# Performance work log

Measured on AMD Instinct MI355X. Metric: run time of the kernel, lower is better.

The kernel has to match this reference:

```python
import jax, jax.numpy as jnp
import numpy as np

B, N, M, K = 128, 128, 16, 8      # graphs, nodes/graph, num_samples, pearl_k
H_MLP = 16                        # pearl_mlp_out
D_PE = 64                         # pe_dims (GIN hidden/out)
E = 262144
BN_EPS = 1e-5


def setup_inputs() -> dict:
    key = jax.random.key(0)
    ks = jax.random.split(key, 16)
    lap = jax.random.normal(ks[0], (B, N, N), dtype=jnp.float32) * 0.1
    W0 = jax.random.normal(ks[1], (B, N, M), dtype=jnp.float32)
    edge_index = jax.random.randint(ks[2], (2, E), 0, B * N, dtype=jnp.int32)
    s = lambda k, sh, fan: jax.random.normal(k, sh, dtype=jnp.float32) / np.sqrt(fan)
    return {
        "lap": lap,
        "W0": W0,
        "mlp_W": s(ks[3], (K, H_MLP), K),
        "mlp_b": jnp.zeros((H_MLP,), jnp.float32),
        "bn_g": jnp.ones((H_MLP,), jnp.float32),
        "bn_b": jnp.zeros((H_MLP,), jnp.float32),
        "eps1": jnp.zeros((), jnp.float32),
        "W1a": s(ks[4], (H_MLP, D_PE), H_MLP),
        "b1a": jnp.zeros((D_PE,), jnp.float32),
        "W1b": s(ks[5], (D_PE, D_PE), D_PE),
        "b1b": jnp.zeros((D_PE,), jnp.float32),
        "eps2": jnp.zeros((), jnp.float32),
        "W2a": s(ks[6], (D_PE, D_PE), D_PE),
        "b2a": jnp.zeros((D_PE,), jnp.float32),
        "W2b": s(ks[7], (D_PE, D_PE), D_PE),
        "b2b": jnp.zeros((D_PE,), jnp.float32),
        "edge_index": edge_index,
    }


def _gin_layer(h, eps, Wa, ba, Wb, bb, src, dst, num_nodes):
    # h: [Nsum, M, D]; GIN aggregation: (1+eps)*h + sum_{j in N(i)} h_j
    agg = jax.ops.segment_sum(h[src], dst, num_segments=num_nodes)
    z = (1.0 + eps) * h + agg
    z = jax.nn.relu(jnp.einsum("nmd,de->nme", z, Wa) + ba)
    z = jnp.einsum("nmd,de->nme", z, Wb) + bb
    return jax.nn.relu(z)


def reference(lap, W0, mlp_W, mlp_b, bn_g, bn_b, eps1, W1a, b1a, W1b, b1b,
              eps2, W2a, b2a, W2b, b2b, edge_index):
    # polynomial filter: stack [W, S@W, S^2@W, ...]  -> [B, N, M, K]
    out = W0
    ws = [out]
    for _ in range(K - 1):
        out = jnp.einsum("bij,bjm->bim", lap, out)
        ws.append(out)
    feat = jnp.stack(ws, axis=-1)                       # [B, N, M, K]

    # per-graph MLP over trailing k dim + BatchNorm1d (training stats, per graph)
    h = jnp.einsum("bnmk,kh->bnmh", feat, mlp_W) + mlp_b  # [B, N, M, H]
    mu = jnp.mean(h, axis=(1, 2), keepdims=True)
    var = jnp.var(h, axis=(1, 2), keepdims=True)
    h = (h - mu) * jax.lax.rsqrt(var + BN_EPS) * bn_g + bn_b
    h = jax.nn.relu(h)

    # concat graphs -> [Nsum, M, H]; GIN over batched edge_index
    h = h.reshape(B * N, M, H_MLP)
    src, dst = edge_index[0], edge_index[1]
    h = _gin_layer(h, eps1, W1a, b1a, W1b, b1b, src, dst, B * N)
    h = _gin_layer(h, eps2, W2a, b2a, W2b, b2b, src, dst, B * N)

    # RandomSampleAggregator: sum over the sample dim -> [Nsum, D_pe]
    return h.sum(axis=1)
```

## Files before the change

### kernel.cpp

```cpp
#include <hip/hip_runtime.h>

typedef unsigned short u16;
typedef unsigned int   u32;
typedef short bf16x8 __attribute__((ext_vector_type(8)));
typedef float f32x4  __attribute__((ext_vector_type(4)));

#define BG    128
#define NN    128
#define MS    16
#define KP    8
#define HM    16
#define DP    64
#define NSUM  16384
#define NE    262144
#define SITES 2048


__device__ __forceinline__ float blo(u32 u){ union{u32 i; float f;} v; v.i=u<<16; return v.f; }
__device__ __forceinline__ float bhi(u32 u){ union{u32 i; float f;} v; v.i=u&0xffff0000u; return v.f; }
__device__ __forceinline__ u16  f2b(float f){ union{float f; u32 i;} v; v.f=f; u32 x=v.i; x += 0x7fffu + ((x>>16)&1u); return (u16)(x>>16); }
__device__ __forceinline__ u32  pk2(float a, float b){ return (u32)f2b(a) | ((u32)f2b(b)<<16); }

__device__ __forceinline__ void fsplit(float x, short& hi, short& lo){
  u16 h = f2b(x); hi = (short)h; lo = (short)f2b(x - blo((u32)h));
}

__device__ __forceinline__ void acc4s(float* a, uint2 x, float s){
  a[0]+=s*blo(x.x); a[1]+=s*bhi(x.x); a[2]+=s*blo(x.y); a[3]+=s*bhi(x.y);
}
__device__ __forceinline__ void acc16s(float* a, uint4 x0, uint4 x1, float s){
  a[0] +=s*blo(x0.x); a[1] +=s*bhi(x0.x); a[2] +=s*blo(x0.y); a[3] +=s*bhi(x0.y);
  a[4] +=s*blo(x0.z); a[5] +=s*bhi(x0.z); a[6] +=s*blo(x0.w); a[7] +=s*bhi(x0.w);
  a[8] +=s*blo(x1.x); a[9] +=s*bhi(x1.x); a[10]+=s*blo(x1.y); a[11]+=s*bhi(x1.y);
  a[12]+=s*blo(x1.z); a[13]+=s*bhi(x1.z); a[14]+=s*blo(x1.w); a[15]+=s*bhi(x1.w);
}

#define MFMA16(a,b,c) __builtin_amdgcn_mfma_f32_16x16x32_bf16(a,b,c,0,0,0)

__device__ __forceinline__ bf16x8 bfragW(const float* __restrict__ W, int nrows,
                                         int k0, int nb, int col, int quad){
  bf16x8 f;
  #pragma unroll
  for(int j=0;j<8;++j){
    int k = k0 + quad*8 + j;
    float v = (k < nrows) ? W[k*DP + nb + col] : 0.f;
    f[j] = (short)f2b(v);
  }
  return f;
}
__device__ __forceinline__ bf16x8 afragT(const float* tp){
  float4 v0 = *(const float4*)tp;
  float4 v1 = *(const float4*)(tp+4);
  bf16x8 a;
  a[0]=(short)f2b(v0.x); a[1]=(short)f2b(v0.y); a[2]=(short)f2b(v0.z); a[3]=(short)f2b(v0.w);
  a[4]=(short)f2b(v1.x); a[5]=(short)f2b(v1.y); a[6]=(short)f2b(v1.z); a[7]=(short)f2b(v1.w);
  return a;
}

__global__ __launch_bounds__(256,1) void k_poly(
    const float* __restrict__ lap, const float* __restrict__ W0, const float* __restrict__ mlpW,
    const float* __restrict__ bng, const float* __restrict__ bnb, u16* __restrict__ h1,
    int* __restrict__ cnt)
{
  __shared__ float Wbuf[2][SITES];
  __shared__ float mlpWS[KP*HM];
  __shared__ float red[4][32];
  __shared__ float stat[32];
  __shared__ float ssc[HM], ssh[HM];

  const int b = blockIdx.x, t = threadIdx.x, l = t&63, w = t>>6;
  const int col = l&15, quad = l>>4;
  if (t < 128) cnt[b*128 + t] = 0;

  {
    const float4* src = (const float4*)(W0 + (size_t)b*SITES);
    for (int i=t; i<SITES/4; i+=256) ((float4*)Wbuf[0])[i] = src[i];
    if (t < KP*HM) mlpWS[t] = mlpW[t];
  }

  bf16x8 Ah[2][4], Al[2][4];
  {
    const float* lg = lap + (size_t)b*NN*NN;
    #pragma unroll
    for(int Mt=0;Mt<2;++Mt){
      const int nr = w*32 + Mt*16 + col;
      #pragma unroll
      for(int Kc=0;Kc<4;++Kc){
        const float* p = lg + (size_t)nr*NN + Kc*32 + quad*8;
        float4 v0 = *(const float4*)p;
        float4 v1 = *(const float4*)(p+4);
        float xs[8] = {v0.x,v0.y,v0.z,v0.w,v1.x,v1.y,v1.z,v1.w};
        #pragma unroll
        for(int j=0;j<8;++j){ short hi,lo; fsplit(xs[j],hi,lo); Ah[Mt][Kc][j]=hi; Al[Mt][Kc][j]=lo; }
      }
    }
  }

  float h[8][16];
  {
    const float* w0g = W0 + (size_t)b*SITES;
    #pragma unroll
    for(int Mt=0;Mt<2;++Mt){
      #pragma unroll
      for(int r=0;r<4;++r){
        const int n = w*32 + Mt*16 + quad*4 + r;
        float sv = w0g[n*MS + col];
        #pragma unroll
        for(int c=0;c<16;++c) h[Mt*4+r][c] = sv*mlpW[c];
      }
    }
  }
  __syncthreads();

  int cur=0;
  for(int k=1;k<KP;++k){
    f32x4 c0 = {0.f,0.f,0.f,0.f};
    f32x4 c1 = {0.f,0.f,0.f,0.f};
    #pragma unroll
    for(int Kc=0;Kc<4;++Kc){
      const float* wb = &Wbuf[cur][(Kc*32 + quad*8)*MS + col];
      bf16x8 Bh, Bl;
      #pragma unroll
      for(int j=0;j<8;++j){
        float x = wb[j*MS];
        short hi,lo; fsplit(x,hi,lo); Bh[j]=hi; Bl[j]=lo;
      }
      c0 = MFMA16(Ah[0][Kc], Bh, c0);
      c0 = MFMA16(Ah[0][Kc], Bl, c0);
      c0 = MFMA16(Al[0][Kc], Bh, c0);
      c1 = MFMA16(Ah[1][Kc], Bh, c1);
      c1 = MFMA16(Ah[1][Kc], Bl, c1);
      c1 = MFMA16(Al[1][Kc], Bh, c1);
    }
    float mw[16];
    #pragma unroll
    for(int c=0;c<16;++c) mw[c]=mlpWS[k*16+c];
    #pragma unroll
    for(int r=0;r<4;++r){
      const int n0 = w*32 + quad*4 + r;
      Wbuf[cur^1][n0*MS + col]        = c0[r];
      Wbuf[cur^1][(n0+16)*MS + col]   = c1[r];
      #pragma unroll
      for(int c=0;c<16;++c){ h[r][c] += c0[r]*mw[c]; h[4+r][c] += c1[r]*mw[c]; }
    }
    __syncthreads();
    cur ^= 1;
  }

  float sum[16], sq[16];
  #pragma unroll
  for(int c=0;c<16;++c){ sum[c]=0.f; sq[c]=0.f; }
  #pragma unroll
  for(int s=0;s<8;++s){
    #pragma unroll
    for(int c=0;c<16;++c){ float v=h[s][c]; sum[c]+=v; sq[c]+=v*v; }
  }
  #pragma unroll
  for(int d=1;d<64;d<<=1){
    #pragma unroll
    for(int c=0;c<16;++c){ sum[c]+=__shfl_xor(sum[c],d,64); sq[c]+=__shfl_xor(sq[c],d,64); }
  }
  if(l==0){
    #pragma unroll
    for(int c=0;c<16;++c){ red[w][c]=sum[c]; red[w][16+c]=sq[c]; }
  }
  __syncthreads();
  if(t<32) stat[t]=red[0][t]+red[1][t]+red[2][t]+red[3][t];
  __syncthreads();
  if(t<16){
    float mu  = stat[t]*(1.f/SITES);
    float var = stat[16+t]*(1.f/SITES) - mu*mu;
    float sc  = bng[t] * rsqrtf(var + 1e-5f);
    ssc[t]=sc; ssh[t]=bnb[t] - mu*sc;
  }
  __syncthreads();
  {
    float sc[16], sh[16];
    #pragma unroll
    for(int c=0;c<16;++c){ sc[c]=ssc[c]; sh[c]=ssh[c]; }
    #pragma unroll
    for(int s=0;s<8;++s){
      const int n = w*32 + (s>>2)*16 + quad*4 + (s&3);
      const int node = b*NN + n;
      float r[16];
      #pragma unroll
      for(int c=0;c<16;++c) r[c]=fmaxf(h[s][c]*sc[c]+sh[c], 0.f);
      uint4 A;
      A.x=pk2(r[0],r[1]);  A.y=pk2(r[2],r[3]);  A.z=pk2(r[4],r[5]);  A.w=pk2(r[6],r[7]);
      uint4 Bv;
      Bv.x=pk2(r[8],r[9]); Bv.y=pk2(r[10],r[11]); Bv.z=pk2(r[12],r[13]); Bv.w=pk2(r[14],r[15]);
      u16* o = h1 + (size_t)node*256 + (size_t)col*HM;
      *(uint4*)o     = A;
      *(uint4*)(o+8) = Bv;
    }
  }
}

__global__ void k_hist(const int* __restrict__ dst, int* __restrict__ cnt){
  int e = blockIdx.x*256 + threadIdx.x;
  atomicAdd(&cnt[dst[e]], 1);
}

__global__ void k_scan(const int* __restrict__ cnt, int* __restrict__ off, int* __restrict__ wpos){
  __shared__ int ps[256];
  const int t = threadIdx.x, PER = NSUM/256;
  int s=0;
  for(int i=0;i<PER;++i) s += cnt[t*PER+i];
  ps[t]=s; __syncthreads();
  for(int d=1; d<256; d<<=1){
    int v = (t>=d) ? ps[t-d] : 0;
    __syncthreads();
    ps[t] += v;
    __syncthreads();
  }
  int run = (t==0) ? 0 : ps[t-1];
  for(int i=0;i<PER;++i){
    int idx=t*PER+i;
    off[idx]=run; wpos[idx]=run;
    run += cnt[idx];
  }
  if(t==255) off[NSUM]=run;
}

__global__ void k_scatter(const int* __restrict__ srcI, const int* __restrict__ dstI,
                          int* __restrict__ wpos, int* __restrict__ srcs){
  int e = blockIdx.x*256 + threadIdx.x;
  int p = atomicAdd(&wpos[dstI[e]], 1);
  srcs[p] = srcI[e];
}

__global__ __launch_bounds__(256) void k_agg1(
  const u16* __restrict__ h1, const float* __restrict__ eps1p,
  const int* __restrict__ off, const int* __restrict__ srcs, u16* __restrict__ z1)
{
  const int t=threadIdx.x, l=t&63;
  const int node = blockIdx.x*4 + (t>>6);
  const float epe = 1.f + eps1p[0];
  float a[4] = {0.f,0.f,0.f,0.f};
  acc4s(a, *(const uint2*)&h1[(size_t)node*256 + l*4], epe);
  int e=off[node]; const int e1=off[node+1];
  for(; e+8<=e1; e+=8){
    int s0=srcs[e],s1=srcs[e+1],s2=srcs[e+2],s3=srcs[e+3];
    int s4=srcs[e+4],s5=srcs[e+5],s6=srcs[e+6],s7=srcs[e+7];
    uint2 r0=*(const uint2*)&h1[(size_t)s0*256 + l*4];
    uint2 r1=*(const uint2*)&h1[(size_t)s1*256 + l*4];
    uint2 r2=*(const uint2*)&h1[(size_t)s2*256 + l*4];
    uint2 r3=*(const uint2*)&h1[(size_t)s3*256 + l*4];
    uint2 r4=*(const uint2*)&h1[(size_t)s4*256 + l*4];
    uint2 r5=*(const uint2*)&h1[(size_t)s5*256 + l*4];
    uint2 r6=*(const uint2*)&h1[(size_t)s6*256 + l*4];
    uint2 r7=*(const uint2*)&h1[(size_t)s7*256 + l*4];
    acc4s(a,r0,1.f); acc4s(a,r1,1.f); acc4s(a,r2,1.f); acc4s(a,r3,1.f);
    acc4s(a,r4,1.f); acc4s(a,r5,1.f); acc4s(a,r6,1.f); acc4s(a,r7,1.f);
  }
  for(; e<e1; ++e){
    uint2 r=*(const uint2*)&h1[(size_t)srcs[e]*256 + l*4];
    acc4s(a,r,1.f);
  }
  uint2 o; o.x=pk2(a[0],a[1]); o.y=pk2(a[2],a[3]);
  *(uint2*)&z1[(size_t)node*256 + l*4] = o;
}

__global__ __launch_bounds__(256) void k_agg2(
  const u16* __restrict__ h2, const float* __restrict__ eps2p,
  const int* __restrict__ off, const int* __restrict__ srcs, u16* __restrict__ z2)
{
  const int t=threadIdx.x, l=t&63;
  const int node = blockIdx.x*4 + (t>>6);
  const float epe = 1.f + eps2p[0];
  float a[16];
  #pragma unroll
  for(int i=0;i<16;++i) a[i]=0.f;
  {
    const uint4* r=(const uint4*)&h2[(size_t)node*1024 + l*16];
    acc16s(a, r[0], r[1], epe);
  }
  int e=off[node]; const int e1=off[node+1];
  for(; e+8<=e1; e+=8){
    int s0=srcs[e],s1=srcs[e+1],s2=srcs[e+2],s3=srcs[e+3];
    int s4=srcs[e+4],s5=srcs[e+5],s6=srcs[e+6],s7=srcs[e+7];
    const uint4* r0=(const uint4*)&h2[(size_t)s0*1024 + l*16];
    const uint4* r1=(const uint4*)&h2[(size_t)s1*1024 + l*16];
    const uint4* r2=(const uint4*)&h2[(size_t)s2*1024 + l*16];
    const uint4* r3=(const uint4*)&h2[(size_t)s3*1024 + l*16];
    const uint4* r4=(const uint4*)&h2[(size_t)s4*1024 + l*16];
    const uint4* r5=(const uint4*)&h2[(size_t)s5*1024 + l*16];
    const uint4* r6=(const uint4*)&h2[(size_t)s6*1024 + l*16];
    const uint4* r7=(const uint4*)&h2[(size_t)s7*1024 + l*16];
    uint4 a0=r0[0],b0=r0[1], a1=r1[0],b1=r1[1], a2=r2[0],b2=r2[1], a3=r3[0],b3=r3[1];
    uint4 a4=r4[0],b4=r4[1], a5=r5[0],b5=r5[1], a6=r6[0],b6=r6[1], a7=r7[0],b7=r7[1];
    acc16s(a,a0,b0,1.f); acc16s(a,a1,b1,1.f); acc16s(a,a2,b2,1.f); acc16s(a,a3,b3,1.f);
    acc16s(a,a4,b4,1.f); acc16s(a,a5,b5,1.f); acc16s(a,a6,b6,1.f); acc16s(a,a7,b7,1.f);
  }
  for(; e<e1; ++e){
    const uint4* r=(const uint4*)&h2[(size_t)srcs[e]*1024 + l*16];
    acc16s(a, r[0], r[1], 1.f);
  }
  uint4 o0, o1;
  o0.x=pk2(a[0],a[1]);   o0.y=pk2(a[2],a[3]);   o0.z=pk2(a[4],a[5]);   o0.w=pk2(a[6],a[7]);
  o1.x=pk2(a[8],a[9]);   o1.y=pk2(a[10],a[11]); o1.z=pk2(a[12],a[13]); o1.w=pk2(a[14],a[15]);
  uint4* zp = (uint4*)&z2[(size_t)node*1024 + l*16];
  zp[0]=o0; zp[1]=o1;
}

__global__ __launch_bounds__(256) void k_mm1(
  const u16* __restrict__ z1, const float* __restrict__ W1a, const float* __restrict__ b1a,
  const float* __restrict__ W1b, const float* __restrict__ b1b, u16* __restrict__ h2)
{
  __shared__ float tS[4][16*68 + 4];
  const int t=threadIdx.x, l=t&63, w=t>>6;
  const int col=l&15, quad=l>>4;

  bf16x8 fa[4], fb[4][2];
  float bav[4], bbv[4];
  #pragma unroll
  for(int nt=0;nt<4;++nt){
    fa[nt]    = bfragW(W1a, HM, 0,  nt*16, col, quad);
    fb[nt][0] = bfragW(W1b, DP, 0,  nt*16, col, quad);
    fb[nt][1] = bfragW(W1b, DP, 32, nt*16, col, quad);
    bav[nt] = b1a[nt*16+col];
    bbv[nt] = b1b[nt*16+col];
  }
  for(int ni=0;ni<2;++ni){
    const int node = blockIdx.x*8 + ni*4 + w;
    bf16x8 a0;
    #pragma unroll
    for(int j=0;j<8;++j) a0[j]=0;
    if (quad < 2) a0 = *(const bf16x8*)&z1[(size_t)node*256 + col*16 + quad*8];
    #pragma unroll
    for(int nt=0;nt<4;++nt){
      f32x4 c = {bav[nt], bav[nt], bav[nt], bav[nt]};
      c = MFMA16(a0, fa[nt], c);
      #pragma unroll
      for(int r=0;r<4;++r)
        tS[w][(quad*4+r)*68 + nt*16 + col] = fmaxf(c[r], 0.f);
    }
    bf16x8 ta0 = afragT(&tS[w][col*68 + quad*8]);
    bf16x8 ta1 = afragT(&tS[w][col*68 + 32 + quad*8]);
    #pragma unroll
    for(int nt=0;nt<4;++nt){
      f32x4 c = {bbv[nt], bbv[nt], bbv[nt], bbv[nt]};
      c = MFMA16(ta0, fb[nt][0], c);
      c = MFMA16(ta1, fb[nt][1], c);
      #pragma unroll
      for(int r=0;r<4;++r)
        h2[(size_t)node*1024 + (quad*4+r)*64 + nt*16 + col] = f2b(fmaxf(c[r], 0.f));
    }
  }
}

__global__ __launch_bounds__(256) void k_mm2(
  const u16* __restrict__ z2, const float* __restrict__ W2a, const float* __restrict__ b2a,
  const float* __restrict__ W2b, const float* __restrict__ b2b, float* __restrict__ out)
{
  __shared__ float tS[4][16*68 + 4];
  const int t=threadIdx.x, l=t&63, w=t>>6;
  const int col=l&15, quad=l>>4;

  bf16x8 fa[4][2], fb[4][2];
  float bav[4], bbv[4];
  #pragma unroll
  for(int nt=0;nt<4;++nt){
    fa[nt][0] = bfragW(W2a, DP, 0,  nt*16, col, quad);
    fa[nt][1] = bfragW(W2a, DP, 32, nt*16, col, quad);
    fb[nt][0] = bfragW(W2b, DP, 0,  nt*16, col, quad);
    fb[nt][1] = bfragW(W2b, DP, 32, nt*16, col, quad);
    bav[nt] = b2a[nt*16+col];
    bbv[nt] = b2b[nt*16+col];
  }
  for(int ni=0;ni<2;++ni){
    const int node = blockIdx.x*8 + ni*4 + w;
    const u16* zrow = &z2[(size_t)node*1024];
    bf16x8 a0 = *(const bf16x8*)&zrow[col*64 + quad*8];
    bf16x8 a1 = *(const bf16x8*)&zrow[col*64 + quad*8 + 32];
    #pragma unroll
    for(int nt=0;nt<4;++nt){
      f32x4 c = {bav[nt], bav[nt], bav[nt], bav[nt]};
      c = MFMA16(a0, fa[nt][0], c);
      c = MFMA16(a1, fa[nt][1], c);
      #pragma unroll
      for(int r=0;r<4;++r)
        tS[w][(quad*4+r)*68 + nt*16 + col] = fmaxf(c[r], 0.f);
    }
    bf16x8 ta0 = afragT(&tS[w][col*68 + quad*8]);
    bf16x8 ta1 = afragT(&tS[w][col*68 + 32 + quad*8]);
    #pragma unroll
    for(int nt=0;nt<4;++nt){
      f32x4 c = {bbv[nt], bbv[nt], bbv[nt], bbv[nt]};
      c = MFMA16(ta0, fb[nt][0], c);
      c = MFMA16(ta1, fb[nt][1], c);
      float s = fmaxf(c[0],0.f)+fmaxf(c[1],0.f)+fmaxf(c[2],0.f)+fmaxf(c[3],0.f);
      s += __shfl_xor(s, 16, 64);
      s += __shfl_xor(s, 32, 64);
      if (quad == 0)
        out[(size_t)node*64 + nt*16 + col] = s;
    }
  }
}

extern "C" void kernel_launch(void* const* d_in, const int* in_sizes, int n_in,
                              void* d_out, int out_size, void* d_ws, size_t ws_size,
                              hipStream_t stream)
{
  (void)in_sizes; (void)n_in; (void)out_size; (void)ws_size;
  const float* lap  = (const float*)d_in[0];
  const float* W0   = (const float*)d_in[1];
  const float* mlpW = (const float*)d_in[2];
  const float* bng  = (const float*)d_in[4];
  const float* bnb  = (const float*)d_in[5];
  const float* eps1 = (const float*)d_in[6];
  const float* W1a  = (const float*)d_in[7];
  const float* b1a  = (const float*)d_in[8];
  const float* W1b  = (const float*)d_in[9];
  const float* b1b  = (const float*)d_in[10];
  const float* eps2 = (const float*)d_in[11];
  const float* W2a  = (const float*)d_in[12];
  const float* b2a  = (const float*)d_in[13];
  const float* W2b  = (const float*)d_in[14];
  const float* b2b  = (const float*)d_in[15];
  const int*   ei   = (const int*)d_in[16];
  const int* srcI = ei;
  const int* dstI = ei + NE;

  char* ws = (char*)d_ws;
  u16* h1   = (u16*)(ws);
  u16* z1   = (u16*)(ws + 8388608);
  u16* h2   = (u16*)(ws + 16777216);
  u16* z2   = (u16*)(ws + 50331648);
  int* cnt  = (int*)(ws + 83886080);
  int* offA = (int*)(ws + 83951616);
  int* wpos = (int*)(ws + 84017408);
  int* srcs = (int*)(ws + 84082944);

  k_poly   <<<BG,      256, 0, stream>>>(lap, W0, mlpW, bng, bnb, h1, cnt);
  k_hist   <<<NE/256,  256, 0, stream>>>(dstI, cnt);
  k_scan   <<<1,       256, 0, stream>>>(cnt, offA, wpos);
  k_scatter<<<NE/256,  256, 0, stream>>>(srcI, dstI, wpos, srcs);
  k_agg1   <<<NSUM/4,  256, 0, stream>>>(h1, eps1, offA, srcs, z1);
  k_mm1    <<<NSUM/8,  256, 0, stream>>>(z1, W1a, b1a, W1b, b1b, h2);
  k_agg2   <<<NSUM/4,  256, 0, stream>>>(h2, eps2, offA, srcs, z2);
  k_mm2    <<<NSUM/8,  256, 0, stream>>>(z2, W2a, b2a, W2b, b2b, (float*)d_out);
}
```

Measured before the change: 282.0 us.

## Store layer-1 GIN output sample-major and gather per-sample slices in agg2

k_mm1 now writes h2 in a sample-major layout [M][Nsum][D], and k_agg2 is restructured so each block handles a single sample index m for 32 nodes. Eight lanes cooperatively gather each 128-byte node slice, and every wave loops to the warp-wide maximum degree with masked contributions. The aim is a smaller working set per block (2 MB per sample slice instead of 32 MB), which should improve L2 locality for the random neighbour gathers. In exchange, mm1 writes become strided, the degree imbalance across each wave is padded with wasted loads, and srcs/offsets are reread 16 times.

```diff
diff --git a/kernel.cpp b/kernel.cpp
--- a/kernel.cpp
+++ b/kernel.cpp
@@ -4,6 +4,7 @@
 typedef unsigned int   u32;
 typedef short bf16x8 __attribute__((ext_vector_type(8)));
 typedef float f32x4  __attribute__((ext_vector_type(4)));
+typedef float f32x2  __attribute__((ext_vector_type(2)));
 
 #define BG    128
 #define NN    128
@@ -20,6 +21,7 @@
 __device__ __forceinline__ float bhi(u32 u){ union{u32 i; float f;} v; v.i=u&0xffff0000u; return v.f; }
 __device__ __forceinline__ u16  f2b(float f){ union{float f; u32 i;} v; v.f=f; u32 x=v.i; x += 0x7fffu + ((x>>16)&1u); return (u16)(x>>16); }
 __device__ __forceinline__ u32  pk2(float a, float b){ return (u32)f2b(a) | ((u32)f2b(b)<<16); }
+__device__ __forceinline__ f32x2 up2(u32 u){ f32x2 v; v.x=blo(u); v.y=bhi(u); return v; }
 
 __device__ __forceinline__ void fsplit(float x, short& hi, short& lo){
   u16 h = f2b(x); hi = (short)h; lo = (short)f2b(x - blo((u32)h));
@@ -27,12 +29,6 @@
 
 __device__ __forceinline__ void acc4s(float* a, uint2 x, float s){
   a[0]+=s*blo(x.x); a[1]+=s*bhi(x.x); a[2]+=s*blo(x.y); a[3]+=s*bhi(x.y);
-}
-__device__ __forceinline__ void acc16s(float* a, uint4 x0, uint4 x1, float s){
-  a[0] +=s*blo(x0.x); a[1] +=s*bhi(x0.x); a[2] +=s*blo(x0.y); a[3] +=s*bhi(x0.y);
-  a[4] +=s*blo(x0.z); a[5] +=s*bhi(x0.z); a[6] +=s*blo(x0.w); a[7] +=s*bhi(x0.w);
-  a[8] +=s*blo(x1.x); a[9] +=s*bhi(x1.x); a[10]+=s*blo(x1.y); a[11]+=s*bhi(x1.y);
-  a[12]+=s*blo(x1.z); a[13]+=s*bhi(x1.z); a[14]+=s*blo(x1.w); a[15]+=s*bhi(x1.w);
 }
 
 #define MFMA16(a,b,c) __builtin_amdgcn_mfma_f32_16x16x32_bf16(a,b,c,0,0,0)
@@ -262,50 +258,60 @@
 }
 
 __global__ __launch_bounds__(256) void k_agg2(
-  const u16* __restrict__ h2, const float* __restrict__ eps2p,
+  const u16* __restrict__ h2T, const float* __restrict__ eps2p,
   const int* __restrict__ off, const int* __restrict__ srcs, u16* __restrict__ z2)
 {
-  const int t=threadIdx.x, l=t&63;
-  const int node = blockIdx.x*4 + (t>>6);
+  const int t=threadIdx.x, l=t&63, w=t>>6;
+  const int m = blockIdx.x & 15, g = blockIdx.x >> 4;
+  const int grp = l>>3, q = l&7;
+  const int node = g*32 + w*8 + grp;
   const float epe = 1.f + eps2p[0];
-  float a[16];
-  #pragma unroll
-  for(int i=0;i<16;++i) a[i]=0.f;
+  const u16* __restrict__ base = h2T + (size_t)m*NSUM*DP;
+
+  f32x2 A[4];
   {
-    const uint4* r=(const uint4*)&h2[(size_t)node*1024 + l*16];
-    acc16s(a, r[0], r[1], epe);
-  }
-  int e=off[node]; const int e1=off[node+1];
-  for(; e+8<=e1; e+=8){
-    int s0=srcs[e],s1=srcs[e+1],s2=srcs[e+2],s3=srcs[e+3];
-    int s4=srcs[e+4],s5=srcs[e+5],s6=srcs[e+6],s7=srcs[e+7];
-    const uint4* r0=(const uint4*)&h2[(size_t)s0*1024 + l*16];
-    const uint4* r1=(const uint4*)&h2[(size_t)s1*1024 + l*16];
-    const uint4* r2=(const uint4*)&h2[(size_t)s2*1024 + l*16];
-    const uint4* r3=(const uint4*)&h2[(size_t)s3*1024 + l*16];
-    const uint4* r4=(const uint4*)&h2[(size_t)s4*1024 + l*16];
-    const uint4* r5=(const uint4*)&h2[(size_t)s5*1024 + l*16];
-    const uint4* r6=(const uint4*)&h2[(size_t)s6*1024 + l*16];
-    const uint4* r7=(const uint4*)&h2[(size_t)s7*1024 + l*16];
-    uint4 a0=r0[0],b0=r0[1], a1=r1[0],b1=r1[1], a2=r2[0],b2=r2[1], a3=r3[0],b3=r3[1];
-    uint4 a4=r4[0],b4=r4[1], a5=r5[0],b5=r5[1], a6=r6[0],b6=r6[1], a7=r7[0],b7=r7[1];
-    acc16s(a,a0,b0,1.f); acc16s(a,a1,b1,1.f); acc16s(a,a2,b2,1.f); acc16s(a,a3,b3,1.f);
-    acc16s(a,a4,b4,1.f); acc16s(a,a5,b5,1.f); acc16s(a,a6,b6,1.f); acc16s(a,a7,b7,1.f);
-  }
-  for(; e<e1; ++e){
-    const uint4* r=(const uint4*)&h2[(size_t)srcs[e]*1024 + l*16];
-    acc16s(a, r[0], r[1], 1.f);
-  }
-  uint4 o0, o1;
-  o0.x=pk2(a[0],a[1]);   o0.y=pk2(a[2],a[3]);   o0.z=pk2(a[4],a[5]);   o0.w=pk2(a[6],a[7]);
-  o1.x=pk2(a[8],a[9]);   o1.y=pk2(a[10],a[11]); o1.z=pk2(a[12],a[13]); o1.w=pk2(a[14],a[15]);
-  uint4* zp = (uint4*)&z2[(size_t)node*1024 + l*16];
-  zp[0]=o0; zp[1]=o1;
+    uint4 x = *(const uint4*)&base[(size_t)node*DP + q*8];
+    f32x2 s2; s2.x=epe; s2.y=epe;
+    A[0]=s2*up2(x.x); A[1]=s2*up2(x.y); A[2]=s2*up2(x.z); A[3]=s2*up2(x.w);
+  }
+  const int e0 = off[node], e1 = off[node+1];
+  int dmax = e1 - e0;
+  #pragma unroll
+  for(int d=1; d<64; d<<=1) dmax = max(dmax, __shfl_xor(dmax, d, 64));
+
+  int i = 0;
+  for(; i+2 <= dmax; i += 2){
+    int pa = e0+i, pb = e0+i+1;
+    float sa = (pa < e1) ? 1.f : 0.f;
+    float sb = (pb < e1) ? 1.f : 0.f;
+    int ea = min(pa, NE-1), eb = min(pb, NE-1);
+    int ia = srcs[ea], ib = srcs[eb];
+    uint4 xa = *(const uint4*)&base[(size_t)ia*DP + q*8];
+    uint4 xb = *(const uint4*)&base[(size_t)ib*DP + q*8];
+    f32x2 va; va.x=sa; va.y=sa;
+    f32x2 vb; vb.x=sb; vb.y=sb;
+    A[0]+=va*up2(xa.x); A[1]+=va*up2(xa.y); A[2]+=va*up2(xa.z); A[3]+=va*up2(xa.w);
+    A[0]+=vb*up2(xb.x); A[1]+=vb*up2(xb.y); A[2]+=vb*up2(xb.z); A[3]+=vb*up2(xb.w);
+  }
+  if(i < dmax){
+    int pa = e0+i;
+    float sa = (pa < e1) ? 1.f : 0.f;
+    int ea = min(pa, NE-1);
+    int ia = srcs[ea];
+    uint4 xa = *(const uint4*)&base[(size_t)ia*DP + q*8];
+    f32x2 va; va.x=sa; va.y=sa;
+    A[0]+=va*up2(xa.x); A[1]+=va*up2(xa.y); A[2]+=va*up2(xa.z); A[3]+=va*up2(xa.w);
+  }
+
+  uint4 o;
+  o.x=pk2(A[0].x,A[0].y); o.y=pk2(A[1].x,A[1].y);
+  o.z=pk2(A[2].x,A[2].y); o.w=pk2(A[3].x,A[3].y);
+  *(uint4*)&z2[(size_t)node*1024 + m*DP + q*8] = o;
 }
 
 __global__ __launch_bounds__(256) void k_mm1(
   const u16* __restrict__ z1, const float* __restrict__ W1a, const float* __restrict__ b1a,
-  const float* __restrict__ W1b, const float* __restrict__ b1b, u16* __restrict__ h2)
+  const float* __restrict__ W1b, const float* __restrict__ b1b, u16* __restrict__ h2T)
 {
   __shared__ float tS[4][16*68 + 4];
   const int t=threadIdx.x, l=t&63, w=t>>6;
@@ -344,7 +350,7 @@
       c = MFMA16(ta1, fb[nt][1], c);
       #pragma unroll
       for(int r=0;r<4;++r)
-        h2[(size_t)node*1024 + (quad*4+r)*64 + nt*16 + col] = f2b(fmaxf(c[r], 0.f));
+        h2T[((size_t)(quad*4+r)*NSUM + node)*DP + nt*16 + col] = f2b(fmaxf(c[r], 0.f));
     }
   }
 }
@@ -425,7 +431,7 @@
   char* ws = (char*)d_ws;
   u16* h1   = (u16*)(ws);
   u16* z1   = (u16*)(ws + 8388608);
-  u16* h2   = (u16*)(ws + 16777216);
+  u16* h2T  = (u16*)(ws + 16777216);
   u16* z2   = (u16*)(ws + 50331648);
   int* cnt  = (int*)(ws + 83886080);
   int* offA = (int*)(ws + 83951616);
@@ -437,7 +443,7 @@
   k_scan   <<<1,       256, 0, stream>>>(cnt, offA, wpos);
   k_scatter<<<NE/256,  256, 0, stream>>>(srcI, dstI, wpos, srcs);
   k_agg1   <<<NSUM/4,  256, 0, stream>>>(h1, eps1, offA, srcs, z1);
-  k_mm1    <<<NSUM/8,  256, 0, stream>>>(z1, W1a, b1a, W1b, b1b, h2);
-  k_agg2   <<<NSUM/4,  256, 0, stream>>>(h2, eps2, offA, srcs, z2);
+  k_mm1    <<<NSUM/8,  256, 0, stream>>>(z1, W1a, b1a, W1b, b1b, h2T);
+  k_agg2   <<<16*(NSUM/32), 256, 0, stream>>>(h2T, eps2, offA, srcs, z2);
   k_mm2    <<<NSUM/8,  256, 0, stream>>>(z2, W2a, b2a, W2b, b2b, (float*)d_out);
 }
```

Result: faster. 257.4 us (-8.7%).
